# Kernel tuning notes

Measured on AMD Instinct MI355X. Metric: run time of the kernel, lower is better.

The kernel has to match this reference:

```python
import jax, jax.numpy as jnp
import numpy as np

M0, M1, H = 128, 64, 8            # scalar mul, vector mul, num heads
AH0, AH1 = 16, 8                  # per-head irreps: 16x0e + 8x1e
D = M0 + 3 * M1                   # 320 node feature dim
DTP0 = M0 + M1                    # 192 scalar channels out of depthwise TP
DTP1 = M0 + 2 * M1                # 256 vector channels out of depthwise TP
WNUM = 2 * M0 + 3 * M1            # 448 TP path weights (uvu, edge mul=1)
RAD_IN, RAD_HID = 32, 64
N_NODES, N_EDGES = 10000, 160000
INV_SQRT3 = 1.0 / np.sqrt(3.0)    # CG norm for 1e x 1e -> 0e
INV_SQRT2 = 1.0 / np.sqrt(2.0)    # CG norm for 1e x 1e -> 1e


def _split(x, m0, m1):
    # e3nn layout: [m0 scalars | m1 vectors * 3 components]
    return x[..., :m0], x[..., m0:].reshape(x.shape[:-1] + (m1, 3))


def _silu(x):
    return x * jax.nn.sigmoid(x)


def _smooth_leaky(x, a=0.2):
    # SmoothLeakyReLU from equiformer
    return 0.5 * (1 + a) * x + 0.5 * (1 - a) * x * (2.0 * jax.nn.sigmoid(x) - 1.0)


def _dtp(s, v, e0, e1, w):
    # depthwise (uvu) tensor product of (M0x0e + M1x1e) with edge attr (1x0e + 1x1e)
    # s [E,M0], v [E,M1,3], e0 [E,1], e1 [E,3], w [E,WNUM] or [WNUM] (internal)
    w1, w2, w3, w4, w5 = jnp.split(w, [M0, 2 * M0, 2 * M0 + M1, 2 * M0 + 2 * M1], axis=-1)
    os1 = w1 * s * e0                                                  # 0e x 0e -> 0e
    os2 = w4 * (jnp.einsum('emc,ec->em', v, e1) * INV_SQRT3)           # 1e x 1e -> 0e
    ov1 = (w2 * s)[..., None] * e1[:, None, :]                         # 0e x 1e -> 1e
    ov2 = w3[..., None] * v * e0[..., None]                            # 1e x 0e -> 1e
    ov3 = w5[..., None] * (jnp.cross(v, e1[:, None, :]) * INV_SQRT2)   # 1e x 1e -> 1e
    return jnp.concatenate([os1, os2], -1), jnp.concatenate([ov1, ov2, ov3], -2)


def _forward(node_input, edge_src, edge_dst, edge_attr, edge_scalars,
             Wsrc_s, Wsrc_v, bsrc, Wdst_s, Wdst_v,
             rad_W1, rad_b1, rad_W2, rad_off,
             Wact_s, bact, Wact_v, Walpha, balpha, w_int,
             Wval_s, bval, Wval_v, alpha_dot, Wproj_s, bproj, Wproj_v):
    N = node_input.shape[0]
    E = edge_src.shape[0]
    s, v = _split(node_input, M0, M1)
    # merge_src / merge_dst: per-irrep linear (bias only on scalars of src)
    ms_s = s @ Wsrc_s + bsrc
    ms_v = jnp.einsum('nmc,mk->nkc', v, Wsrc_v)
    md_s = s @ Wdst_s
    md_v = jnp.einsum('nmc,mk->nkc', v, Wdst_v)
    msg_s = ms_s[edge_src] + md_s[edge_dst]          # [E, M0]
    msg_v = ms_v[edge_src] + md_v[edge_dst]          # [E, M1, 3]
    e0, e1 = edge_attr[:, :1], edge_attr[:, 1:4]
    # radial profile MLP -> edge-dependent TP weights
    w = _silu(edge_scalars @ rad_W1 + rad_b1) @ rad_W2 + rad_off       # [E, WNUM]
    ds, dv = _dtp(msg_s, msg_v, e0, e1, w)           # [E, DTP0], [E, DTP1, 3]
    # alpha branch: linear on TP scalars -> heads -> smooth leaky -> dot
    al = _smooth_leaky((ds @ Walpha + balpha).reshape(E, H, AH0))
    logits = jnp.einsum('ehk,hk->eh', al, alpha_dot[0])                # [E, H]
    # value branch: sep_act.lin + gate
    scal = ds @ Wact_s + bact                        # [E, M0+M1] scalars+gates
    gated_v = jnp.einsum('emc,mk->ekc', dv, Wact_v)  # [E, M1, 3]
    val_s = _silu(scal[:, :M0])
    val_v = gated_v * jax.nn.sigmoid(scal[:, M0:])[..., None]
    # sep_value: depthwise TP with internal weights + linear
    vs, vv = _dtp(val_s, val_v, e0, e1, w_int)
    out_s = vs @ Wval_s + bval                       # [E, H*AH0]
    out_v = jnp.einsum('emc,mk->ekc', vv, Wval_v)    # [E, H*AH1, 3]
    value = jnp.concatenate([out_s.reshape(E, H, AH0),
                             out_v.reshape(E, H, AH1 * 3)], axis=2)    # [E, H, 40]
    # softmax over incoming edges per destination node
    mx = jax.lax.stop_gradient(jax.ops.segment_max(logits, edge_dst, num_segments=N))
    mx = jnp.where(jnp.isfinite(mx), mx, 0.0)
    ex = jnp.exp(logits - mx[edge_dst])
    den = jax.ops.segment_sum(ex, edge_dst, num_segments=N)
    alpha = ex / (den[edge_dst] + 1e-16)             # [E, H]
    agg = jax.ops.segment_sum(value * alpha[..., None], edge_dst, num_segments=N)
    # heads2vec + output projection
    node_s = agg[:, :, :AH0].reshape(N, H * AH0)
    node_v = agg[:, :, AH0:].reshape(N, H * AH1, 3)
    po_s = node_s @ Wproj_s + bproj
    po_v = jnp.einsum('nmc,mk->nkc', node_v, Wproj_v)
    return jnp.concatenate([po_s, po_v.reshape(N, M1 * 3)], axis=1)


def _lin(key, fi, fo):
    return jax.random.normal(key, (fi, fo), jnp.float32) / np.sqrt(fi)


def setup_inputs() -> dict:
    ks = iter(jax.random.split(jax.random.key(0), 40))
    inp = {}
    inp['node_input'] = jax.random.normal(next(ks), (N_NODES, D), jnp.float32)
    inp['edge_src'] = jax.random.randint(next(ks), (N_EDGES,), 0, N_NODES)
    inp['edge_dst'] = jax.random.randint(next(ks), (N_EDGES,), 0, N_NODES)
    inp['edge_attr'] = jax.random.normal(next(ks), (N_EDGES, 4), jnp.float32)
    inp['edge_scalars'] = jax.random.normal(next(ks), (N_EDGES, RAD_IN), jnp.float32)
    inp['Wsrc_s'] = _lin(next(ks), M0, M0)
    inp['Wsrc_v'] = _lin(next(ks), M1, M1)
    inp['bsrc'] = 0.1 * jax.random.normal(next(ks), (M0,), jnp.float32)
    inp['Wdst_s'] = _lin(next(ks), M0, M0)
    inp['Wdst_v'] = _lin(next(ks), M1, M1)
    inp['rad_W1'] = _lin(next(ks), RAD_IN, RAD_HID)
    inp['rad_b1'] = 0.1 * jax.random.normal(next(ks), (RAD_HID,), jnp.float32)
    inp['rad_W2'] = _lin(next(ks), RAD_HID, WNUM)
    inp['rad_off'] = 0.1 * jax.random.normal(next(ks), (WNUM,), jnp.float32)
    inp['Wact_s'] = _lin(next(ks), DTP0, M0 + M1)
    inp['bact'] = 0.1 * jax.random.normal(next(ks), (M0 + M1,), jnp.float32)
    inp['Wact_v'] = _lin(next(ks), DTP1, M1)
    inp['Walpha'] = _lin(next(ks), DTP0, H * AH0)
    inp['balpha'] = 0.1 * jax.random.normal(next(ks), (H * AH0,), jnp.float32)
    inp['w_int'] = jax.random.normal(next(ks), (WNUM,), jnp.float32)
    inp['Wval_s'] = _lin(next(ks), DTP0, H * AH0)
    inp['bval'] = 0.1 * jax.random.normal(next(ks), (H * AH0,), jnp.float32)
    inp['Wval_v'] = _lin(next(ks), DTP1, H * AH1)
    inp['alpha_dot'] = jax.random.normal(next(ks), (1, H, AH0), jnp.float32) / np.sqrt(AH0)
    inp['Wproj_s'] = _lin(next(ks), H * AH0, M0)
    inp['bproj'] = 0.1 * jax.random.normal(next(ks), (M0,), jnp.float32)
    inp['Wproj_v'] = _lin(next(ks), H * AH1, M1)
    return inp


def reference(node_input, edge_src, edge_dst, edge_attr, edge_scalars,
              Wsrc_s, Wsrc_v, bsrc, Wdst_s, Wdst_v,
              rad_W1, rad_b1, rad_W2, rad_off,
              Wact_s, bact, Wact_v, Walpha, balpha, w_int,
              Wval_s, bval, Wval_v, alpha_dot, Wproj_s, bproj, Wproj_v):
    return _forward(node_input, edge_src, edge_dst, edge_attr, edge_scalars,
                    Wsrc_s, Wsrc_v, bsrc, Wdst_s, Wdst_v,
                    rad_W1, rad_b1, rad_W2, rad_off,
                    Wact_s, bact, Wact_v, Walpha, balpha, w_int,
                    Wval_s, bval, Wval_v, alpha_dot, Wproj_s, bproj, Wproj_v)
```

## Files before the change

kernel.cpp:

```cpp
#include <hip/hip_runtime.h>

#define NN 10000
#define NE 160000
#define INV_SQRT3f 0.57735026918962576f
#define INV_SQRT2f 0.70710678118654752f
#define VPLU 640000

typedef short bshort8 __attribute__((ext_vector_type(8)));
typedef float floatx4 __attribute__((ext_vector_type(4)));
#define MFMA16(a,b,c) __builtin_amdgcn_mfma_f32_16x16x32_bf16((a),(b),(c),0,0,0)

__device__ __forceinline__ float sigm(float x){ return 1.f/(1.f+__expf(-x)); }
__device__ __forceinline__ float siluf(float x){ return x*sigm(x); }
__device__ __forceinline__ float sleaky(float x){ return 0.6f*x + 0.4f*x*(2.f*sigm(x)-1.f); }
__device__ __forceinline__ unsigned short f2bf(float f){
  return (unsigned short)((__float_as_uint(f) + 0x8000u)>>16);
}
__device__ __forceinline__ float bf2f(unsigned short h){
  return __uint_as_float(((unsigned)h)<<16);
}
__device__ __forceinline__ unsigned cvtpk(float lo, float hi){
  unsigned r;
  asm("v_cvt_pk_bf16_f32 %0, %1, %2" : "=v"(r) : "v"(lo), "v"(hi));
  return r;
}
__device__ __forceinline__ float lo16f(unsigned u){ return __uint_as_float(u<<16); }
__device__ __forceinline__ float hi16f(unsigned u){ return __uint_as_float(u & 0xffff0000u); }

#define O_W1   0
#define O_W2   2048
#define O_WAS  30720
#define O_WAVT 67584
#define O_WAVB 75776
#define O_WVS  83968
#define O_WVVT 108544
#define O_WVVB 116736
#define O_WALP 124928
#define SWZ_TOTAL 149504

__global__ __launch_bounds__(256) void k_pre_all(
    const float* __restrict__ x,
    const float* __restrict__ Wsrc_s, const float* __restrict__ Wsrc_v,
    const float* __restrict__ bsrc,
    const float* __restrict__ Wdst_s, const float* __restrict__ Wdst_v,
    unsigned short* __restrict__ ms_s, unsigned short* __restrict__ md_s,
    unsigned short* __restrict__ ms_v, unsigned short* __restrict__ md_v,
    const float* __restrict__ W1, const float* __restrict__ W2,
    const float* __restrict__ WAs, const float* __restrict__ WAv,
    const float* __restrict__ WVs, const float* __restrict__ WVv,
    const float* __restrict__ WAl, const float* __restrict__ w_int,
    unsigned short* __restrict__ swz,
    float* __restrict__ num, float* __restrict__ den, int* __restrict__ cnt) {
  __shared__ __align__(16) float s_s[128*16];
  __shared__ __align__(16) float s_v[192*16];
  const int tid = threadIdx.x;
  const int b = blockIdx.x;
  if (b >= 1209) {
    int base = (b-1209)*256 + tid;
    float4 z = {0.f,0.f,0.f,0.f};
    for (int i = base; i < 800000; i += 554496) ((float4*)num)[i] = z;
    if (base < 20000) ((float4*)den)[base] = z;
    if (base < 10000) cnt[base] = 0;
    return;
  }
  if (b >= 625) {
    int s = (b-625)*256 + tid;
    if (s >= SWZ_TOTAL) return;
    const float* src; int base, N, KT, rowOff;
    if      (s < 2048)  { base=O_W1;   src=W1;  N=64;  KT=1; rowOff=0; }
    else if (s < 30720) { base=O_W2;   src=W2;  N=448; KT=2; rowOff=0; }
    else if (s < 67584) { base=O_WAS;  src=WAs; N=192; KT=6; rowOff=0; }
    else if (s < 75776) { base=O_WAVT; src=WAv; N=64;  KT=4; rowOff=0; }
    else if (s < 83968) { base=O_WAVB; src=WAv; N=64;  KT=4; rowOff=128; }
    else if (s < 108544){ base=O_WVS;  src=WVs; N=128; KT=6; rowOff=0; }
    else if (s < 116736){ base=O_WVVT; src=WVv; N=64;  KT=4; rowOff=0; }
    else if (s < 124928){ base=O_WVVB; src=WVv; N=64;  KT=4; rowOff=128; }
    else                { base=O_WALP; src=WAl; N=128; KT=6; rowOff=0; }
    int loc = s - base;
    int j = loc & 7, l = (loc>>3)&63, kt = (loc>>9)%KT, nt = loc/(512*KT);
    int row = kt*32 + (l>>4)*8 + j + rowOff;
    int col = nt*16 + (l&15);
    float scl = 1.f;
    if      (base == O_WVS)  scl = (row < 128) ? w_int[row] : w_int[192+row]*INV_SQRT3f;
    else if (base == O_WVVT) scl = w_int[128+row];
    else if (base == O_WVVB) scl = (row < 192) ? w_int[128+row] : w_int[192+row]*INV_SQRT2f;
    swz[s] = f2bf(src[row*N + col] * scl);
    return;
  }
  const int n0 = b*16;
  for (int idx = tid; idx < 16*320; idx += 256) {
    int n = idx/320, d = idx - n*320;
    float val = x[(n0+n)*320 + d];
    if (d < 128) s_s[d*16+n] = val;
    else         s_v[(d-128)*16+n] = val;
  }
  __syncthreads();
  {
    int g = tid>>7, j = tid&127;
    float accs[8], accd[8];
    float bb = bsrc[j];
    #pragma unroll
    for (int i=0;i<8;i++){ accs[i]=bb; accd[i]=0.f; }
    for (int k=0;k<128;k++) {
      float w1 = Wsrc_s[k*128+j], w2 = Wdst_s[k*128+j];
      float4 a0 = *(const float4*)&s_s[k*16+g*8];
      float4 a1 = *(const float4*)&s_s[k*16+g*8+4];
      accs[0]+=a0.x*w1; accs[1]+=a0.y*w1; accs[2]+=a0.z*w1; accs[3]+=a0.w*w1;
      accs[4]+=a1.x*w1; accs[5]+=a1.y*w1; accs[6]+=a1.z*w1; accs[7]+=a1.w*w1;
      accd[0]+=a0.x*w2; accd[1]+=a0.y*w2; accd[2]+=a0.z*w2; accd[3]+=a0.w*w2;
      accd[4]+=a1.x*w2; accd[5]+=a1.y*w2; accd[6]+=a1.z*w2; accd[7]+=a1.w*w2;
    }
    #pragma unroll
    for (int i=0;i<8;i++){ int n=n0+g*8+i; ms_s[n*128+j]=f2bf(accs[i]); md_s[n*128+j]=f2bf(accd[i]); }
  }
  if (tid < 192) {
    int c = tid>>6, k = tid&63;
    #pragma unroll
    for (int half=0; half<2; ++half) {
      float accs[8], accd[8];
      #pragma unroll
      for (int e=0;e<8;e++){ accs[e]=0.f; accd[e]=0.f; }
      for (int m=0;m<64;m++) {
        float w1 = Wsrc_v[m*64+k], w2 = Wdst_v[m*64+k];
        float4 v0 = *(const float4*)&s_v[(m*3+c)*16 + half*8];
        float4 v1 = *(const float4*)&s_v[(m*3+c)*16 + half*8 + 4];
        accs[0]+=v0.x*w1; accs[1]+=v0.y*w1; accs[2]+=v0.z*w1; accs[3]+=v0.w*w1;
        accs[4]+=v1.x*w1; accs[5]+=v1.y*w1; accs[6]+=v1.z*w1; accs[7]+=v1.w*w1;
        accd[0]+=v0.x*w2; accd[1]+=v0.y*w2; accd[2]+=v0.z*w2; accd[3]+=v0.w*w2;
        accd[4]+=v1.x*w2; accd[5]+=v1.y*w2; accd[6]+=v1.z*w2; accd[7]+=v1.w*w2;
      }
      #pragma unroll
      for (int e=0;e<8;e++){
        int n = n0 + half*8 + e;
        ms_v[c*VPLU + n*64 + k] = f2bf(accs[e]);
        md_v[c*VPLU + n*64 + k] = f2bf(accd[e]);
      }
    }
  }
}

__global__ __launch_bounds__(256) void k_hist(const int* __restrict__ edst,
                                              int* __restrict__ cnt) {
  int e = blockIdx.x*256 + threadIdx.x;
  if (e < NE) atomicAdd(&cnt[edst[e]], 1);
}

__global__ __launch_bounds__(256) void k_scan(const int* __restrict__ cnt,
                                              int* __restrict__ offs) {
  __shared__ int sc[10240];
  __shared__ int wsum[4];
  const int tid = threadIdx.x;
  const int lane = tid & 63, wave = tid >> 6;
  for (int i = tid; i < 10240; i += 256) sc[i] = (i < NN) ? cnt[i] : 0;
  __syncthreads();
  int v[40]; int s = 0;
  #pragma unroll
  for (int j=0;j<40;j++){ v[j] = sc[tid*40+j]; s += v[j]; }
  int incl = s;
  #pragma unroll
  for (int d=1; d<64; d<<=1) { int t = __shfl_up(incl, d, 64); if (lane>=d) incl += t; }
  if (lane==63) wsum[wave] = incl;
  __syncthreads();
  int wbase = 0;
  for (int w=0; w<wave; ++w) wbase += wsum[w];
  int excl = wbase + incl - s;
  #pragma unroll
  for (int j=0;j<40;j++){ int i = tid*40+j; if (i<NN) offs[i] = excl; excl += v[j]; }
}

__global__ __launch_bounds__(256) void k_scatter(const int* __restrict__ edst,
                                                 int* __restrict__ offs,
                                                 int* __restrict__ perm) {
  int e = blockIdx.x*256 + threadIdx.x;
  if (e < NE) {
    int pos = atomicAdd(&offs[edst[e]], 1);
    perm[pos] = e;
  }
}

__global__ __launch_bounds__(256, 5) void e_all(
    const unsigned short* __restrict__ ms_s, const unsigned short* __restrict__ md_s,
    const unsigned short* __restrict__ ms_v, const unsigned short* __restrict__ md_v,
    const int* __restrict__ esrc, const int* __restrict__ edst,
    const int* __restrict__ perm,
    const float* __restrict__ eattr, const float* __restrict__ escal,
    const float* __restrict__ rad_b1, const float* __restrict__ rad_off,
    const float* __restrict__ bact,
    const float* __restrict__ bval,
    const float* __restrict__ balpha, const float* __restrict__ alpha_dot,
    const unsigned short* __restrict__ swz,
    float* __restrict__ den, float* __restrict__ num) {
  __shared__ __align__(16) char smem[30912];
  unsigned short* sw_v = (unsigned short*)smem;
  float* vout          = (float*)smem;
  unsigned short* ads  = (unsigned short*)(smem+6144);
  unsigned short* at1  = (unsigned short*)(smem+12544);
  unsigned short* advb = (unsigned short*)(smem+16896);
  unsigned short* aes  = (unsigned short*)(smem+16896);
  unsigned short* ah   = (unsigned short*)(smem+19456);
  float* s_e0 = (float*)(smem+29952);
  float* s_e1 = (float*)(smem+30016);
  float* s_ex = (float*)(smem+30208);
  int* s_eid  = (int*)(smem+30720);
  int* s_src  = (int*)(smem+30784);
  int* s_dst  = (int*)(smem+30848);
  const int tid  = threadIdx.x;
  const int lane = tid & 63, wave = tid >> 6;
  const int quad = lane >> 4, l15 = lane & 15;
  const int bswz = (blockIdx.x & 7)*1250 + (blockIdx.x >> 3);
  const int eb = bswz*16;

  if (tid < 16) {
    int eid = perm[eb+tid];
    s_eid[tid] = eid; s_src[tid] = esrc[eid]; s_dst[tid] = edst[eid];
  }
  __syncthreads();
  if (tid >= 64 && tid < 128) {
    int t = tid-64, e = t>>2, q = t&3;
    float a = eattr[s_eid[e]*4+q];
    if (q == 0) s_e0[e] = a; else s_e1[(q-1)*16+e] = a;
  }
  {
    int e = tid>>4, i0 = (tid&15)*2;
    float2 es = *(const float2*)&escal[s_eid[e]*32+i0];
    *(unsigned*)&aes[e*40+i0] = cvtpk(es.x, es.y);
  }
  __syncthreads();

  {
    int nt = wave, col = nt*16 + l15;
    bshort8 a = *(const bshort8*)&aes[l15*40 + quad*8];
    bshort8 b = *(const bshort8*)&swz[O_W1 + (nt*64 + lane)*8];
    float bb = rad_b1[col];
    floatx4 acc = {bb,bb,bb,bb};
    acc = MFMA16(a, b, acc);
    #pragma unroll
    for (int r=0;r<4;r++) ah[(quad*4+r)*72 + col] = f2bf(siluf(acc[r]));
  }
  __syncthreads();

  {
    bshort8 ha0 = *(const bshort8*)&ah[l15*72 + quad*8];
    bshort8 ha1 = *(const bshort8*)&ah[l15*72 + 32 + quad*8];
    int src_[4], dst_[4];
    #pragma unroll
    for (int r=0;r<4;r++){ int e=quad*4+r; src_[r]=s_src[e]; dst_[r]=s_dst[e]; }
    #pragma unroll
    for (int p=0;p<2;p++) {
      int nt1 = wave*2+p, nt2 = nt1+8;
      int m = nt1*16 + l15;
      float o1 = rad_off[m], o2 = rad_off[128+m];
      floatx4 a1 = {o1,o1,o1,o1}, a2 = {o2,o2,o2,o2};
      a1 = MFMA16(ha0, *(const bshort8*)&swz[O_W2 + ((nt1*2+0)*64+lane)*8], a1);
      a1 = MFMA16(ha1, *(const bshort8*)&swz[O_W2 + ((nt1*2+1)*64+lane)*8], a1);
      a2 = MFMA16(ha0, *(const bshort8*)&swz[O_W2 + ((nt2*2+0)*64+lane)*8], a2);
      a2 = MFMA16(ha1, *(const bshort8*)&swz[O_W2 + ((nt2*2+1)*64+lane)*8], a2);
      #pragma unroll
      for (int r=0;r<4;r++) {
        int e = quad*4+r;
        float msgs = bf2f(ms_s[src_[r]*128+m]) + bf2f(md_s[dst_[r]*128+m]);
        ads[e*200+m] = f2bf(a1[r]*msgs*s_e0[e]);
        at1[e*136+m] = f2bf(a2[r]*msgs);
      }
    }
    #pragma unroll
    for (int q=0;q<3;q++) {
      int nt = 16 + wave*3 + q, col = nt*16 + l15;
      float o = rad_off[col];
      floatx4 acc = {o,o,o,o};
      acc = MFMA16(ha0, *(const bshort8*)&swz[O_W2 + ((nt*2+0)*64+lane)*8], acc);
      acc = MFMA16(ha1, *(const bshort8*)&swz[O_W2 + ((nt*2+1)*64+lane)*8], acc);
      #pragma unroll
      for (int r=0;r<4;r++) sw_v[(quad*4+r)*192 + (col-256)] = f2bf(acc[r]);
    }
  }
  __syncthreads();

  #pragma unroll
  for (int it = 0; it < 2; ++it) {
    int t = tid + it*256;
    int e = t>>5, pr = t&31;
    int k0 = pr*2;
    int sb = s_src[e]*64 + k0, db = s_dst[e]*64 + k0;
    unsigned usx = *(const unsigned*)&ms_v[0*VPLU+sb];
    unsigned usy = *(const unsigned*)&ms_v[1*VPLU+sb];
    unsigned usz = *(const unsigned*)&ms_v[2*VPLU+sb];
    unsigned udx = *(const unsigned*)&md_v[0*VPLU+db];
    unsigned udy = *(const unsigned*)&md_v[1*VPLU+db];
    unsigned udz = *(const unsigned*)&md_v[2*VPLU+db];
    unsigned uw3 = *(const unsigned*)&sw_v[e*192 + k0];
    unsigned uw4 = *(const unsigned*)&sw_v[e*192 + 64 + k0];
    unsigned uw5 = *(const unsigned*)&sw_v[e*192 + 128 + k0];
    float ex1 = s_e1[0+e], ey1 = s_e1[16+e], ez1 = s_e1[32+e];
    float e0 = s_e0[e];
    float vx0 = lo16f(usx)+lo16f(udx), vx1 = hi16f(usx)+hi16f(udx);
    float vy0 = lo16f(usy)+lo16f(udy), vy1 = hi16f(usy)+hi16f(udy);
    float vz0 = lo16f(usz)+lo16f(udz), vz1 = hi16f(usz)+hi16f(udz);
    float d0 = vx0*ex1 + vy0*ey1 + vz0*ez1;
    float d1 = vx1*ex1 + vy1*ey1 + vz1*ez1;
    *(unsigned*)&ads[e*200+128+k0] =
        cvtpk(lo16f(uw4)*d0*INV_SQRT3f, hi16f(uw4)*d1*INV_SQRT3f);
    float w30 = lo16f(uw3)*e0, w31 = hi16f(uw3)*e0;
    float w50 = lo16f(uw5)*INV_SQRT2f, w51 = hi16f(uw5)*INV_SQRT2f;
    *(unsigned*)&advb[0*2176 + e*136 + k0] = cvtpk(w30*vx0, w31*vx1);
    *(unsigned*)&advb[1*2176 + e*136 + k0] = cvtpk(w30*vy0, w31*vy1);
    *(unsigned*)&advb[2*2176 + e*136 + k0] = cvtpk(w30*vz0, w31*vz1);
    *(unsigned*)&advb[0*2176 + e*136 + 64+k0] =
        cvtpk(w50*(vy0*ez1 - vz0*ey1), w51*(vy1*ez1 - vz1*ey1));
    *(unsigned*)&advb[1*2176 + e*136 + 64+k0] =
        cvtpk(w50*(vz0*ex1 - vx0*ez1), w51*(vz1*ex1 - vx1*ez1));
    *(unsigned*)&advb[2*2176 + e*136 + 64+k0] =
        cvtpk(w50*(vx0*ey1 - vy0*ex1), w51*(vx1*ey1 - vy1*ex1));
  }
  __syncthreads();

  floatx4 sc0, sc1, sc2, gsa, gb0, gb1, gb2;
  {
    bshort8 fa[6];
    #pragma unroll
    for (int kt=0;kt<6;kt++) fa[kt] = *(const bshort8*)&ads[l15*200 + kt*32 + quad*8];
    #pragma unroll
    for (int t=0;t<2;t++) {
      int h = wave*2 + t;
      int col = h*16 + l15;
      float bb = balpha[col];
      floatx4 acc = {bb,bb,bb,bb};
      #pragma unroll
      for (int kt=0;kt<6;kt++)
        acc = MFMA16(fa[kt], *(const bshort8*)&swz[O_WALP + ((h*6+kt)*64+lane)*8], acc);
      float ad = alpha_dot[col];
      float exv[4];
      #pragma unroll
      for (int r=0;r<4;r++) {
        float p = sleaky(acc[r])*ad;
        p += __shfl_xor(p, 1);
        p += __shfl_xor(p, 2);
        p += __shfl_xor(p, 4);
        p += __shfl_xor(p, 8);
        float ex = __expf(p);
        exv[r] = ex;
        if (l15 == 0) s_ex[(quad*4+r)*8+h] = ex;
      }
      if (l15 == 0) {
        float racc = exv[0]; int cur = s_dst[quad*4];
        #pragma unroll
        for (int r=1;r<4;r++) {
          int d = s_dst[quad*4+r];
          if (d != cur) { atomicAdd(&den[cur*8+h], racc); racc = 0.f; cur = d; }
          racc += exv[r];
        }
        atomicAdd(&den[cur*8+h], racc);
      }
    }
    {
      float bb = bact[wave*16 + l15];
      floatx4 a0 = {bb,bb,bb,bb};
      #pragma unroll
      for (int kt=0;kt<6;kt++)
        a0 = MFMA16(fa[kt], *(const bshort8*)&swz[O_WAS + ((wave*6+kt)*64+lane)*8], a0);
      sc0 = a0;
    }
    {
      float bb = bact[(wave+4)*16 + l15];
      floatx4 a1 = {bb,bb,bb,bb};
      #pragma unroll
      for (int kt=0;kt<6;kt++)
        a1 = MFMA16(fa[kt], *(const bshort8*)&swz[O_WAS + (((wave+4)*6+kt)*64+lane)*8], a1);
      sc1 = a1;
    }
    {
      float bb = bact[(wave+8)*16 + l15];
      floatx4 a2 = {bb,bb,bb,bb};
      #pragma unroll
      for (int kt=0;kt<6;kt++)
        a2 = MFMA16(fa[kt], *(const bshort8*)&swz[O_WAS + (((wave+8)*6+kt)*64+lane)*8], a2);
      sc2 = a2;
    }
    bshort8 ft[4];
    #pragma unroll
    for (int kt=0;kt<4;kt++) ft[kt] = *(const bshort8*)&at1[l15*136 + kt*32 + quad*8];
    {
      floatx4 acc = {0.f,0.f,0.f,0.f};
      #pragma unroll
      for (int kt=0;kt<4;kt++)
        acc = MFMA16(ft[kt], *(const bshort8*)&swz[O_WAVT + ((wave*4+kt)*64+lane)*8], acc);
      gsa = acc;
    }
    {
      bshort8 wb[4];
      #pragma unroll
      for (int kt=0;kt<4;kt++) wb[kt] = *(const bshort8*)&swz[O_WAVB + ((wave*4+kt)*64+lane)*8];
      #pragma unroll
      for (int c=0;c<3;c++) {
        floatx4 acc = {0.f,0.f,0.f,0.f};
        #pragma unroll
        for (int kt=0;kt<4;kt++) {
          bshort8 fb = *(const bshort8*)&advb[c*2176 + l15*136 + kt*32 + quad*8];
          acc = MFMA16(fb, wb[kt], acc);
        }
        if (c==0) gb0 = acc; else if (c==1) gb1 = acc; else gb2 = acc;
      }
    }
  }
  __syncthreads();

  {
    const int k = wave*16 + l15;
    #pragma unroll
    for (int r=0;r<4;r++) {
      int row = quad*4 + r;
      float e0 = s_e0[row];
      {
        float v = siluf(sc0[r]);
        ads[row*200+k] = f2bf(v*e0);
        at1[row*136+k] = f2bf(v);
      }
      {
        float v = siluf(sc1[r]);
        ads[row*200+64+k] = f2bf(v*e0);
        at1[row*136+64+k] = f2bf(v);
      }
      {
        float sg = sigm(sc2[r]);
        float gs = gsa[r];
        float ex1 = s_e1[0+row], ey1 = s_e1[16+row], ez1 = s_e1[32+row];
        float v0 = (gs*ex1 + gb0[r])*sg;
        float v1 = (gs*ey1 + gb1[r])*sg;
        float v2 = (gs*ez1 + gb2[r])*sg;
        float d = v0*ex1 + v1*ey1 + v2*ez1;
        ads[row*200+128+k] = f2bf(d);
        advb[0*2176 + row*136 + k] = f2bf(v0*e0);
        advb[1*2176 + row*136 + k] = f2bf(v1*e0);
        advb[2*2176 + row*136 + k] = f2bf(v2*e0);
        advb[0*2176 + row*136 + 64+k] = f2bf(v1*ez1 - v2*ey1);
        advb[1*2176 + row*136 + 64+k] = f2bf(v2*ex1 - v0*ez1);
        advb[2*2176 + row*136 + 64+k] = f2bf(v0*ey1 - v1*ex1);
      }
    }
  }
  __syncthreads();

  {
    bshort8 fa[6];
    #pragma unroll
    for (int kt=0;kt<6;kt++) fa[kt] = *(const bshort8*)&ads[l15*200 + kt*32 + quad*8];
    __syncthreads();
    #pragma unroll
    for (int t=0;t<2;t++) {
      int h = wave + 4*t;
      float bb = bval[h*16 + l15];
      floatx4 acc = {bb,bb,bb,bb};
      #pragma unroll
      for (int kt=0;kt<6;kt++)
        acc = MFMA16(fa[kt], *(const bshort8*)&swz[O_WVS + ((h*6+kt)*64+lane)*8], acc);
      #pragma unroll
      for (int r=0;r<4;r++) {
        int row = quad*4 + r;
        vout[row*132 + h*16 + l15] = acc[r]*s_ex[row*8+h];
      }
    }
  }
  __syncthreads();

  if (tid < 128) {
    const int j = tid, h = j>>4, jj = j&15;
    float acc = 0.f; int cur = s_dst[0];
    #pragma unroll
    for (int e = 0; e < 16; ++e) {
      int d = s_dst[e];
      if (d != cur) { atomicAdd(&num[cur*320 + h*40 + jj], acc); acc = 0.f; cur = d; }
      acc += vout[e*132 + j];
    }
    atomicAdd(&num[cur*320 + h*40 + jj], acc);
  }
  __syncthreads();

  {
    bshort8 ft[4];
    #pragma unroll
    for (int kt=0;kt<4;kt++) ft[kt] = *(const bshort8*)&at1[l15*136 + kt*32 + quad*8];
    floatx4 vsh = {0.f,0.f,0.f,0.f};
    #pragma unroll
    for (int kt=0;kt<4;kt++)
      vsh = MFMA16(ft[kt], *(const bshort8*)&swz[O_WVVT + ((wave*4+kt)*64+lane)*8], vsh);
    const int k = wave*16 + l15;
    const int h = k>>3, q = k&7;
    floatx4 vb0, vb1, vb2;
    {
      bshort8 wb[4];
      #pragma unroll
      for (int kt=0;kt<4;kt++) wb[kt] = *(const bshort8*)&swz[O_WVVB + ((wave*4+kt)*64+lane)*8];
      #pragma unroll
      for (int c=0;c<3;c++) {
        floatx4 acc = {0.f,0.f,0.f,0.f};
        #pragma unroll
        for (int kt=0;kt<4;kt++) {
          bshort8 fb = *(const bshort8*)&advb[c*2176 + l15*136 + kt*32 + quad*8];
          acc = MFMA16(fb, wb[kt], acc);
        }
        if (c==0) vb0 = acc; else if (c==1) vb1 = acc; else vb2 = acc;
      }
    }
    #pragma unroll
    for (int r=0;r<4;r++) {
      int row = quad*4 + r;
      float exr = s_ex[row*8+h];
      vout[row*194 + h*24 + q*3 + 0] = (vb0[r] + s_e1[0*16+row]*vsh[r])*exr;
      vout[row*194 + h*24 + q*3 + 1] = (vb1[r] + s_e1[1*16+row]*vsh[r])*exr;
      vout[row*194 + h*24 + q*3 + 2] = (vb2[r] + s_e1[2*16+row]*vsh[r])*exr;
    }
  }
  __syncthreads();

  if (tid < 192) {
    const int jj = tid;
    const int h = jj/24, rr = jj - h*24;
    float acc = 0.f; int cur = s_dst[0];
    #pragma unroll
    for (int e = 0; e < 16; ++e) {
      int d = s_dst[e];
      if (d != cur) { atomicAdd(&num[cur*320 + h*40 + 16 + rr], acc); acc = 0.f; cur = d; }
      acc += vout[e*194 + jj];
    }
    atomicAdd(&num[cur*320 + h*40 + 16 + rr], acc);
  }
}

__global__ __launch_bounds__(256) void node_post(
    const float* __restrict__ num, const float* __restrict__ den,
    const float* __restrict__ Wproj_s, const float* __restrict__ bproj,
    const float* __restrict__ Wproj_v, float* __restrict__ out) {
  __shared__ __align__(16) float s_ns[128*16];
  __shared__ __align__(16) float s_nv[192*16];
  const int tid = threadIdx.x;
  const int n0 = blockIdx.x*16;
  for (int idx = tid; idx < 16*320; idx += 256) {
    int n = idx/320, j = idx - n*320;
    int h = j/40, r = j - h*40;
    float a = num[(n0+n)*320+j] / (den[(n0+n)*8+h] + 1e-16f);
    if (r < 16) s_ns[(h*16+r)*16+n] = a;
    else        s_nv[(h*24 + (r-16))*16+n] = a;
  }
  __syncthreads();
  {
    int g = tid>>7, j = tid&127;
    float acc[8]; float b = bproj[j];
    #pragma unroll
    for (int i=0;i<8;i++) acc[i]=b;
    for (int k=0;k<128;k++) {
      float wv = Wproj_s[k*128+j];
      float4 a0 = *(const float4*)&s_ns[k*16+g*8];
      float4 a1 = *(const float4*)&s_ns[k*16+g*8+4];
      acc[0]+=a0.x*wv; acc[1]+=a0.y*wv; acc[2]+=a0.z*wv; acc[3]+=a0.w*wv;
      acc[4]+=a1.x*wv; acc[5]+=a1.y*wv; acc[6]+=a1.z*wv; acc[7]+=a1.w*wv;
    }
    #pragma unroll
    for (int i=0;i<8;i++) out[(n0+g*8+i)*320 + j] = acc[i];
  }
  if (tid < 192) {
    int c = tid>>6, k = tid&63;
    #pragma unroll
    for (int half=0; half<2; ++half) {
      float acc[8];
      #pragma unroll
      for (int e=0;e<8;e++) acc[e]=0.f;
      for (int m=0;m<64;m++) {
        float wv = Wproj_v[m*64+k];
        float4 v0 = *(const float4*)&s_nv[(m*3+c)*16 + half*8];
        float4 v1 = *(const float4*)&s_nv[(m*3+c)*16 + half*8 + 4];
        acc[0]+=v0.x*wv; acc[1]+=v0.y*wv; acc[2]+=v0.z*wv; acc[3]+=v0.w*wv;
        acc[4]+=v1.x*wv; acc[5]+=v1.y*wv; acc[6]+=v1.z*wv; acc[7]+=v1.w*wv;
      }
      #pragma unroll
      for (int e=0;e<8;e++) out[(n0+half*8+e)*320 + 128 + k*3 + c] = acc[e];
    }
  }
}

extern "C" void kernel_launch(void* const* d_in, const int* in_sizes, int n_in,
                              void* d_out, int out_size, void* d_ws, size_t ws_size,
                              hipStream_t stream) {
  (void)in_sizes; (void)n_in; (void)out_size; (void)ws_size;
  const float* node_input = (const float*)d_in[0];
  const int*   esrc       = (const int*)d_in[1];
  const int*   edst       = (const int*)d_in[2];
  const float* eattr      = (const float*)d_in[3];
  const float* escal      = (const float*)d_in[4];
  const float* Wsrc_s     = (const float*)d_in[5];
  const float* Wsrc_v     = (const float*)d_in[6];
  const float* bsrc       = (const float*)d_in[7];
  const float* Wdst_s     = (const float*)d_in[8];
  const float* Wdst_v     = (const float*)d_in[9];
  const float* rad_W1     = (const float*)d_in[10];
  const float* rad_b1     = (const float*)d_in[11];
  const float* rad_W2     = (const float*)d_in[12];
  const float* rad_off    = (const float*)d_in[13];
  const float* Wact_s     = (const float*)d_in[14];
  const float* bact       = (const float*)d_in[15];
  const float* Wact_v     = (const float*)d_in[16];
  const float* Walpha     = (const float*)d_in[17];
  const float* balpha     = (const float*)d_in[18];
  const float* w_int      = (const float*)d_in[19];
  const float* Wval_s     = (const float*)d_in[20];
  const float* bval       = (const float*)d_in[21];
  const float* Wval_v     = (const float*)d_in[22];
  const float* alpha_dot  = (const float*)d_in[23];
  const float* Wproj_s    = (const float*)d_in[24];
  const float* bproj      = (const float*)d_in[25];
  const float* Wproj_v    = (const float*)d_in[26];
  float* out = (float*)d_out;

  char* wsb = (char*)d_ws;
  unsigned short* ms_s16 = (unsigned short*)(wsb);
  unsigned short* md_s16 = (unsigned short*)(wsb + 2560000);
  unsigned short* ms_v16 = (unsigned short*)(wsb + 5120000);
  unsigned short* md_v16 = (unsigned short*)(wsb + 8960000);
  float* den             = (float*)(wsb + 12800000);
  float* num             = (float*)(wsb + 13120000);
  unsigned short* swz    = (unsigned short*)(wsb + 25920000);
  int* cnt  = (int*)(wsb + 26220032);
  int* offs = (int*)(wsb + 26260032);
  int* perm = (int*)(wsb + 26300032);

  k_pre_all<<<3375, 256, 0, stream>>>(node_input, Wsrc_s, Wsrc_v, bsrc, Wdst_s, Wdst_v,
                                      ms_s16, md_s16, ms_v16, md_v16,
                                      rad_W1, rad_W2, Wact_s, Wact_v, Wval_s, Wval_v,
                                      Walpha, w_int, swz, num, den, cnt);
  k_hist<<<625, 256, 0, stream>>>(edst, cnt);
  k_scan<<<1, 256, 0, stream>>>(cnt, offs);
  k_scatter<<<625, 256, 0, stream>>>(edst, offs, perm);
  e_all<<<10000, 256, 0, stream>>>(ms_s16, md_s16, ms_v16, md_v16, esrc, edst, perm, eattr, escal,
                                   rad_b1, rad_off, bact, bval,
                                   balpha, alpha_dot, swz, den, num);
  node_post<<<625, 256, 0, stream>>>(num, den, Wproj_s, bproj, Wproj_v, out);
}
```

Measured before the change: 382.3 us.

## Fuse scan into scatter kernel and widen per-thread vector TP loads

The single-block scan and the scatter kernel are merged. Each of the 625 blocks now recomputes the full 10000-entry exclusive scan in shared memory and then places its edges using a separately zeroed per-node rank counter. This drops one kernel launch and the serial dependency on a one-block kernel, at the cost of redundant scan work in every block. Separately, the vector tensor-product stage in e_all now has each thread handle 4 channels with 8-byte loads in one pass, instead of 2 channels over two iterations.

```diff
diff --git a/kernel.cpp b/kernel.cpp
--- a/kernel.cpp
+++ b/kernel.cpp
@@ -50,7 +50,8 @@
     const float* __restrict__ WVs, const float* __restrict__ WVv,
     const float* __restrict__ WAl, const float* __restrict__ w_int,
     unsigned short* __restrict__ swz,
-    float* __restrict__ num, float* __restrict__ den, int* __restrict__ cnt) {
+    float* __restrict__ num, float* __restrict__ den,
+    int* __restrict__ cnt, int* __restrict__ rank) {
   __shared__ __align__(16) float s_s[128*16];
   __shared__ __align__(16) float s_v[192*16];
   const int tid = threadIdx.x;
@@ -60,7 +61,7 @@
     float4 z = {0.f,0.f,0.f,0.f};
     for (int i = base; i < 800000; i += 554496) ((float4*)num)[i] = z;
     if (base < 20000) ((float4*)den)[base] = z;
-    if (base < 10000) cnt[base] = 0;
+    if (base < 10000) { cnt[base] = 0; rank[base] = 0; }
     return;
   }
   if (b >= 625) {
@@ -145,8 +146,9 @@
   if (e < NE) atomicAdd(&cnt[edst[e]], 1);
 }
 
-__global__ __launch_bounds__(256) void k_scan(const int* __restrict__ cnt,
-                                              int* __restrict__ offs) {
+__global__ __launch_bounds__(256) void k_scan_scatter(
+    const int* __restrict__ cnt, int* __restrict__ rank,
+    const int* __restrict__ edst, int* __restrict__ perm) {
   __shared__ int sc[10240];
   __shared__ int wsum[4];
   const int tid = threadIdx.x;
@@ -165,16 +167,13 @@
   for (int w=0; w<wave; ++w) wbase += wsum[w];
   int excl = wbase + incl - s;
   #pragma unroll
-  for (int j=0;j<40;j++){ int i = tid*40+j; if (i<NN) offs[i] = excl; excl += v[j]; }
-}
-
-__global__ __launch_bounds__(256) void k_scatter(const int* __restrict__ edst,
-                                                 int* __restrict__ offs,
-                                                 int* __restrict__ perm) {
-  int e = blockIdx.x*256 + threadIdx.x;
+  for (int j=0;j<40;j++){ sc[tid*40+j] = excl; excl += v[j]; }
+  __syncthreads();
+  int e = blockIdx.x*256 + tid;
   if (e < NE) {
-    int pos = atomicAdd(&offs[edst[e]], 1);
-    perm[pos] = e;
+    int d = edst[e];
+    int r = atomicAdd(&rank[d], 1);
+    perm[sc[d] + r] = e;
   }
 }
 
@@ -276,41 +275,45 @@
   }
   __syncthreads();
 
-  #pragma unroll
-  for (int it = 0; it < 2; ++it) {
-    int t = tid + it*256;
-    int e = t>>5, pr = t&31;
-    int k0 = pr*2;
+  {
+    const int e = tid>>4, k0 = (tid&15)*4;
     int sb = s_src[e]*64 + k0, db = s_dst[e]*64 + k0;
-    unsigned usx = *(const unsigned*)&ms_v[0*VPLU+sb];
-    unsigned usy = *(const unsigned*)&ms_v[1*VPLU+sb];
-    unsigned usz = *(const unsigned*)&ms_v[2*VPLU+sb];
-    unsigned udx = *(const unsigned*)&md_v[0*VPLU+db];
-    unsigned udy = *(const unsigned*)&md_v[1*VPLU+db];
-    unsigned udz = *(const unsigned*)&md_v[2*VPLU+db];
-    unsigned uw3 = *(const unsigned*)&sw_v[e*192 + k0];
-    unsigned uw4 = *(const unsigned*)&sw_v[e*192 + 64 + k0];
-    unsigned uw5 = *(const unsigned*)&sw_v[e*192 + 128 + k0];
-    float ex1 = s_e1[0+e], ey1 = s_e1[16+e], ez1 = s_e1[32+e];
-    float e0 = s_e0[e];
-    float vx0 = lo16f(usx)+lo16f(udx), vx1 = hi16f(usx)+hi16f(udx);
-    float vy0 = lo16f(usy)+lo16f(udy), vy1 = hi16f(usy)+hi16f(udy);
-    float vz0 = lo16f(usz)+lo16f(udz), vz1 = hi16f(usz)+hi16f(udz);
-    float d0 = vx0*ex1 + vy0*ey1 + vz0*ez1;
-    float d1 = vx1*ex1 + vy1*ey1 + vz1*ez1;
-    *(unsigned*)&ads[e*200+128+k0] =
-        cvtpk(lo16f(uw4)*d0*INV_SQRT3f, hi16f(uw4)*d1*INV_SQRT3f);
-    float w30 = lo16f(uw3)*e0, w31 = hi16f(uw3)*e0;
-    float w50 = lo16f(uw5)*INV_SQRT2f, w51 = hi16f(uw5)*INV_SQRT2f;
-    *(unsigned*)&advb[0*2176 + e*136 + k0] = cvtpk(w30*vx0, w31*vx1);
-    *(unsigned*)&advb[1*2176 + e*136 + k0] = cvtpk(w30*vy0, w31*vy1);
-    *(unsigned*)&advb[2*2176 + e*136 + k0] = cvtpk(w30*vz0, w31*vz1);
-    *(unsigned*)&advb[0*2176 + e*136 + 64+k0] =
-        cvtpk(w50*(vy0*ez1 - vz0*ey1), w51*(vy1*ez1 - vz1*ey1));
-    *(unsigned*)&advb[1*2176 + e*136 + 64+k0] =
-        cvtpk(w50*(vz0*ex1 - vx0*ez1), w51*(vz1*ex1 - vx1*ez1));
-    *(unsigned*)&advb[2*2176 + e*136 + 64+k0] =
-        cvtpk(w50*(vx0*ey1 - vy0*ex1), w51*(vx1*ey1 - vy1*ex1));
+    uint2 usx = *(const uint2*)&ms_v[0*VPLU+sb];
+    uint2 usy = *(const uint2*)&ms_v[1*VPLU+sb];
+    uint2 usz = *(const uint2*)&ms_v[2*VPLU+sb];
+    uint2 udx = *(const uint2*)&md_v[0*VPLU+db];
+    uint2 udy = *(const uint2*)&md_v[1*VPLU+db];
+    uint2 udz = *(const uint2*)&md_v[2*VPLU+db];
+    uint2 uw3 = *(const uint2*)&sw_v[e*192 + k0];
+    uint2 uw4 = *(const uint2*)&sw_v[e*192 + 64 + k0];
+    uint2 uw5 = *(const uint2*)&sw_v[e*192 + 128 + k0];
+    const float ex1 = s_e1[0+e], ey1 = s_e1[16+e], ez1 = s_e1[32+e];
+    const float e0 = s_e0[e];
+    unsigned ax[2]={usx.x,usx.y}, ay[2]={usy.x,usy.y}, az[2]={usz.x,usz.y};
+    unsigned bx[2]={udx.x,udx.y}, by[2]={udy.x,udy.y}, bz[2]={udz.x,udz.y};
+    unsigned w3[2]={uw3.x,uw3.y}, w4[2]={uw4.x,uw4.y}, w5[2]={uw5.x,uw5.y};
+    #pragma unroll
+    for (int p=0;p<2;p++) {
+      const int kk = k0 + 2*p;
+      float vx0 = lo16f(ax[p])+lo16f(bx[p]), vx1 = hi16f(ax[p])+hi16f(bx[p]);
+      float vy0 = lo16f(ay[p])+lo16f(by[p]), vy1 = hi16f(ay[p])+hi16f(by[p]);
+      float vz0 = lo16f(az[p])+lo16f(bz[p]), vz1 = hi16f(az[p])+hi16f(bz[p]);
+      float d0 = vx0*ex1 + vy0*ey1 + vz0*ez1;
+      float d1 = vx1*ex1 + vy1*ey1 + vz1*ez1;
+      *(unsigned*)&ads[e*200+128+kk] =
+          cvtpk(lo16f(w4[p])*d0*INV_SQRT3f, hi16f(w4[p])*d1*INV_SQRT3f);
+      float w30 = lo16f(w3[p])*e0, w31 = hi16f(w3[p])*e0;
+      float w50 = lo16f(w5[p])*INV_SQRT2f, w51 = hi16f(w5[p])*INV_SQRT2f;
+      *(unsigned*)&advb[0*2176 + e*136 + kk] = cvtpk(w30*vx0, w31*vx1);
+      *(unsigned*)&advb[1*2176 + e*136 + kk] = cvtpk(w30*vy0, w31*vy1);
+      *(unsigned*)&advb[2*2176 + e*136 + kk] = cvtpk(w30*vz0, w31*vz1);
+      *(unsigned*)&advb[0*2176 + e*136 + 64+kk] =
+          cvtpk(w50*(vy0*ez1 - vz0*ey1), w51*(vy1*ez1 - vz1*ey1));
+      *(unsigned*)&advb[1*2176 + e*136 + 64+kk] =
+          cvtpk(w50*(vz0*ex1 - vx0*ez1), w51*(vz1*ex1 - vx1*ez1));
+      *(unsigned*)&advb[2*2176 + e*136 + 64+kk] =
+          cvtpk(w50*(vx0*ey1 - vy0*ex1), w51*(vx1*ey1 - vy1*ex1));
+    }
   }
   __syncthreads();
 
@@ -619,16 +622,15 @@
   float* num             = (float*)(wsb + 13120000);
   unsigned short* swz    = (unsigned short*)(wsb + 25920000);
   int* cnt  = (int*)(wsb + 26220032);
-  int* offs = (int*)(wsb + 26260032);
+  int* rank = (int*)(wsb + 26260032);
   int* perm = (int*)(wsb + 26300032);
 
   k_pre_all<<<3375, 256, 0, stream>>>(node_input, Wsrc_s, Wsrc_v, bsrc, Wdst_s, Wdst_v,
                                       ms_s16, md_s16, ms_v16, md_v16,
                                       rad_W1, rad_W2, Wact_s, Wact_v, Wval_s, Wval_v,
-                                      Walpha, w_int, swz, num, den, cnt);
+                                      Walpha, w_int, swz, num, den, cnt, rank);
   k_hist<<<625, 256, 0, stream>>>(edst, cnt);
-  k_scan<<<1, 256, 0, stream>>>(cnt, offs);
-  k_scatter<<<625, 256, 0, stream>>>(edst, offs, perm);
+  k_scan_scatter<<<625, 256, 0, stream>>>(cnt, rank, edst, perm);
   e_all<<<10000, 256, 0, stream>>>(ms_s16, md_s16, ms_v16, md_v16, esrc, edst, perm, eattr, escal,
                                    rad_b1, rad_off, bact, bval,
                                    balpha, alpha_dot, swz, den, num);
```

After: 375.8 us. No clear change (-1.7%).

## Fold histogram into pre kernel and merge scan with scatter

Applied to the files above, without the earlier changes.

The edge-destination histogram moves into extra blocks of the preprocessing kernel, with counts zeroed by a memset. The single-block scan and the scatter become one 625-block kernel in which every block recomputes the full prefix sum in shared memory and then scatters, using a separate rank counter array. This removes two kernel launches and their serialization. In exchange each block repeats the 10000-element scan, and it relies on cnt and rank being contiguous so that one 80000-byte memset zeroes both.

```diff
diff --git a/kernel.cpp b/kernel.cpp
--- a/kernel.cpp
+++ b/kernel.cpp
@@ -50,17 +50,22 @@
     const float* __restrict__ WVs, const float* __restrict__ WVv,
     const float* __restrict__ WAl, const float* __restrict__ w_int,
     unsigned short* __restrict__ swz,
-    float* __restrict__ num, float* __restrict__ den, int* __restrict__ cnt) {
+    const int* __restrict__ edst, int* __restrict__ cnt,
+    float* __restrict__ num, float* __restrict__ den) {
   __shared__ __align__(16) float s_s[128*16];
   __shared__ __align__(16) float s_v[192*16];
   const int tid = threadIdx.x;
   const int b = blockIdx.x;
-  if (b >= 1209) {
-    int base = (b-1209)*256 + tid;
+  if (b >= 1834) {
+    int base = (b-1834)*256 + tid;
     float4 z = {0.f,0.f,0.f,0.f};
     for (int i = base; i < 800000; i += 554496) ((float4*)num)[i] = z;
     if (base < 20000) ((float4*)den)[base] = z;
-    if (base < 10000) cnt[base] = 0;
+    return;
+  }
+  if (b >= 1209) {
+    int e = (b-1209)*256 + tid;
+    if (e < NE) atomicAdd(&cnt[edst[e]], 1);
     return;
   }
   if (b >= 625) {
@@ -139,14 +144,9 @@
   }
 }
 
-__global__ __launch_bounds__(256) void k_hist(const int* __restrict__ edst,
-                                              int* __restrict__ cnt) {
-  int e = blockIdx.x*256 + threadIdx.x;
-  if (e < NE) atomicAdd(&cnt[edst[e]], 1);
-}
-
-__global__ __launch_bounds__(256) void k_scan(const int* __restrict__ cnt,
-                                              int* __restrict__ offs) {
+__global__ __launch_bounds__(256) void k_scan_scatter(
+    const int* __restrict__ cnt, int* __restrict__ rank,
+    const int* __restrict__ edst, int* __restrict__ perm) {
   __shared__ int sc[10240];
   __shared__ int wsum[4];
   const int tid = threadIdx.x;
@@ -165,16 +165,13 @@
   for (int w=0; w<wave; ++w) wbase += wsum[w];
   int excl = wbase + incl - s;
   #pragma unroll
-  for (int j=0;j<40;j++){ int i = tid*40+j; if (i<NN) offs[i] = excl; excl += v[j]; }
-}
-
-__global__ __launch_bounds__(256) void k_scatter(const int* __restrict__ edst,
-                                                 int* __restrict__ offs,
-                                                 int* __restrict__ perm) {
-  int e = blockIdx.x*256 + threadIdx.x;
+  for (int j=0;j<40;j++){ sc[tid*40+j] = excl; excl += v[j]; }
+  __syncthreads();
+  int e = blockIdx.x*256 + tid;
   if (e < NE) {
-    int pos = atomicAdd(&offs[edst[e]], 1);
-    perm[pos] = e;
+    int d = edst[e];
+    int r = atomicAdd(&rank[d], 1);
+    perm[sc[d] + r] = e;
   }
 }
 
@@ -619,16 +616,15 @@
   float* num             = (float*)(wsb + 13120000);
   unsigned short* swz    = (unsigned short*)(wsb + 25920000);
   int* cnt  = (int*)(wsb + 26220032);
-  int* offs = (int*)(wsb + 26260032);
+  int* rank = (int*)(wsb + 26260032);
   int* perm = (int*)(wsb + 26300032);
 
-  k_pre_all<<<3375, 256, 0, stream>>>(node_input, Wsrc_s, Wsrc_v, bsrc, Wdst_s, Wdst_v,
+  hipMemsetAsync(cnt, 0, 80000, stream);
+  k_pre_all<<<4000, 256, 0, stream>>>(node_input, Wsrc_s, Wsrc_v, bsrc, Wdst_s, Wdst_v,
                                       ms_s16, md_s16, ms_v16, md_v16,
                                       rad_W1, rad_W2, Wact_s, Wact_v, Wval_s, Wval_v,
-                                      Walpha, w_int, swz, num, den, cnt);
-  k_hist<<<625, 256, 0, stream>>>(edst, cnt);
-  k_scan<<<1, 256, 0, stream>>>(cnt, offs);
-  k_scatter<<<625, 256, 0, stream>>>(edst, offs, perm);
+                                      Walpha, w_int, swz, edst, cnt, num, den);
+  k_scan_scatter<<<625, 256, 0, stream>>>(cnt, rank, edst, perm);
   e_all<<<10000, 256, 0, stream>>>(ms_s16, md_s16, ms_v16, md_v16, esrc, edst, perm, eattr, escal,
                                    rad_b1, rad_off, bact, bval,
                                    balpha, alpha_dot, swz, den, num);
```

New measurement: 375.5 us (median of 2 runs). About the same (-1.8%).
